# Kernel optimization log

Hardware: AMD Instinct MI355X
Metric: run time of the kernel (lower is better)

## Reference

```python
import jax, jax.numpy as jnp
import numpy as np

B, S, D, H, HD, L, VOCAB, EXP = 32, 744, 512, 8, 64, 4, 1000, 4
EPS = 1e-5


def make_pe(seq_len, d):
    # pe[pos, i]   = sin(pos / 10000**(2*i/d))      (i even)
    # pe[pos, i+1] = cos(pos / 10000**(2*(i+1)/d))  (i even)
    pe = np.zeros((seq_len, d), dtype=np.float32)
    pos = np.arange(seq_len, dtype=np.float32)[:, None]
    i = np.arange(0, d, 2, dtype=np.float32)
    pe[:, 0::2] = np.sin(pos / np.power(10000.0, 2.0 * i / d))
    pe[:, 1::2] = np.cos(pos / np.power(10000.0, 2.0 * (i + 1.0) / d))
    return jnp.asarray(pe)


def setup_inputs() -> dict:
    key = jax.random.key(0)
    ks = jax.random.split(key, 12)
    s = 0.02
    return {
        "x": jax.random.randint(ks[0], (1, B, S), 0, VOCAB, dtype=jnp.int64)
            if jax.config.jax_enable_x64 else jax.random.randint(ks[0], (1, B, S), 0, VOCAB, dtype=jnp.int32),
        "emb": jax.random.normal(ks[1], (VOCAB, D), jnp.float32) * s,
        "pe": make_pe(S, D),
        "Wq": jax.random.normal(ks[2], (L, HD, HD), jnp.float32) * s,
        "Wk": jax.random.normal(ks[3], (L, HD, HD), jnp.float32) * s,
        "Wv": jax.random.normal(ks[4], (L, HD, HD), jnp.float32) * s,
        "Wo": jax.random.normal(ks[5], (L, D, D), jnp.float32) * s,
        "bo": jnp.zeros((L, D), jnp.float32),
        "ln1_w": jnp.ones((L, D), jnp.float32),
        "ln1_b": jnp.zeros((L, D), jnp.float32),
        "W1": jax.random.normal(ks[6], (L, EXP * D, D), jnp.float32) * s,
        "b1": jnp.zeros((L, EXP * D), jnp.float32),
        "W2": jax.random.normal(ks[7], (L, D, EXP * D), jnp.float32) * s,
        "b2": jnp.zeros((L, D), jnp.float32),
        "ln2_w": jnp.ones((L, D), jnp.float32),
        "ln2_b": jnp.zeros((L, D), jnp.float32),
    }


def _layer_norm(x, w, b):
    m = jnp.mean(x, axis=-1, keepdims=True)
    v = jnp.mean(jnp.square(x - m), axis=-1, keepdims=True)
    return (x - m) * jax.lax.rsqrt(v + EPS) * w + b


def _block(h, Wq, Wk, Wv, Wo, bo, g1, be1, W1, bf1, W2, bf2, g2, be2):
    # h: [B, S, D]
    x4 = h.reshape(B, S, H, HD)
    # per-head Linear(64,64, bias=False): y = x @ W.T
    q = jnp.einsum('bshd,ed->bhse', x4, Wq)  # [B,H,S,HD]
    k = jnp.einsum('bshd,ed->bhse', x4, Wk)
    v = jnp.einsum('bshd,ed->bhse', x4, Wv)
    scores = jnp.einsum('bhse,bhte->bhst', q, k) / jnp.sqrt(jnp.float32(HD))
    att = jax.nn.softmax(scores, axis=-1)
    o = jnp.einsum('bhst,bhte->bshe', att, v).reshape(B, S, D)
    o = o @ Wo.T + bo
    # residual uses `value` == h (pre-attention input)
    n1 = _layer_norm(o + h, g1, be1)  # dropout is identity in eval
    ff = jax.nn.relu(n1 @ W1.T + bf1) @ W2.T + bf2
    return _layer_norm(ff + n1, g2, be2)


def reference(x, emb, pe, Wq, Wk, Wv, Wo, bo, ln1_w, ln1_b, W1, b1, W2, b2, ln2_w, ln2_b):
    # embedding + [0, ...] -> [B, S, D]
    h = emb[x][0]
    h = h * jnp.sqrt(jnp.float32(D)) + pe  # pe broadcast over batch
    for l in range(L):
        h = _block(h, Wq[l], Wk[l], Wv[l], Wo[l], bo[l],
                   ln1_w[l], ln1_b[l], W1[l], b1[l], W2[l], b2[l],
                   ln2_w[l], ln2_b[l])
    return h
```

## Files before the change

kernel.cpp:

```cpp
#include <hip/hip_runtime.h>
#include <hip/hip_bf16.h>
#include <math.h>

#define BB 32
#define SS 744
#define DD 512
#define HH 8
#define HDD 64
#define LL 4
#define EXPAND 4
#define NROWS (BB * SS)
#define MROWS (NROWS * HH)
#define NBUF ((size_t)NROWS * DD)
#define SQRT_D 22.62741699796952f
#define QSCALE 0.18033688011112042f
#define VTS 768

typedef __hip_bfloat16 bf16;
typedef __attribute__((ext_vector_type(8))) __bf16 bf16x8;
typedef __attribute__((ext_vector_type(4))) float f32x4;

#define GPTR(p) (const __attribute__((address_space(1))) void*)(p)
#define LPTR(p) (__attribute__((address_space(3))) void*)(p)


__global__ __launch_bounds__(128) void k_embed(const int* __restrict__ x,
                                               const float* __restrict__ emb,
                                               const float* __restrict__ pe,
                                               float* __restrict__ h,
                                               bf16* __restrict__ h16) {
    int row = blockIdx.x;
    int s = row % SS;
    int tok = x[row];
    int t = threadIdx.x;
    float4 e = ((const float4*)(emb + (size_t)tok * DD))[t];
    float4 p = ((const float4*)(pe + (size_t)s * DD))[t];
    float4 o;
    o.x = e.x * SQRT_D + p.x;
    o.y = e.y * SQRT_D + p.y;
    o.z = e.z * SQRT_D + p.z;
    o.w = e.w * SQRT_D + p.w;
    ((float4*)(h + (size_t)row * DD))[t] = o;
    bf16 b0 = __float2bfloat16(o.x), b1 = __float2bfloat16(o.y);
    bf16 b2 = __float2bfloat16(o.z), b3 = __float2bfloat16(o.w);
    ushort4 u;
    u.x = *(unsigned short*)&b0; u.y = *(unsigned short*)&b1;
    u.z = *(unsigned short*)&b2; u.w = *(unsigned short*)&b3;
    ((ushort4*)(h16 + (size_t)row * DD))[t] = u;
}

__global__ __launch_bounds__(256) void k_f2b(const float* __restrict__ in,
                                             bf16* __restrict__ out, int n) {
    for (int i = blockIdx.x * 256 + threadIdx.x; i < n; i += gridDim.x * 256)
        out[i] = __float2bfloat16(in[i]);
}

__global__ __launch_bounds__(256) void k_qkv_mfma(const bf16* __restrict__ A,
                                                  const bf16* __restrict__ Wqkv,
                                                  bf16* __restrict__ qk,
                                                  bf16* __restrict__ v) {
    __shared__ __align__(16) bf16 As[2][128][32];
    __shared__ __align__(16) bf16 Ws[2][192][32];
    int t = threadIdx.x;
    int w = t >> 6, lane = t & 63;
    int fr = lane & 15, fq = lane >> 4;
    int m0 = blockIdx.x * 128;
    int wm = (w >> 1) * 64;
    int wc = (w & 1) * 96;
    int lr = lane >> 2;
    int csw = ((lane & 3) ^ ((lane >> 3) & 3)) * 8;
    int swz8 = (fq ^ ((fr >> 1) & 3)) * 8;

#pragma unroll
    for (int kc = 0; kc < 2; kc++)
#pragma unroll
        for (int i = 0; i < 2; i++) {
            int rb = w * 32 + i * 16;
            __builtin_amdgcn_global_load_lds(
                GPTR(A + (size_t)(m0 + rb + lr) * 64 + kc * 32 + csw),
                LPTR(&As[kc][rb][0]), 16, 0, 0);
        }
#pragma unroll
    for (int kc = 0; kc < 2; kc++)
#pragma unroll
        for (int i = 0; i < 3; i++) {
            int rb = w * 48 + i * 16;
            __builtin_amdgcn_global_load_lds(
                GPTR(Wqkv + (size_t)(rb + lr) * 64 + kc * 32 + csw),
                LPTR(&Ws[kc][rb][0]), 16, 0, 0);
        }
    __syncthreads();

    bf16x8 af[2][4], bw[2][6];
#pragma unroll
    for (int kc = 0; kc < 2; kc++) {
#pragma unroll
        for (int mi = 0; mi < 4; mi++)
            af[kc][mi] = *(const bf16x8*)&As[kc][wm + mi * 16 + fr][swz8];
#pragma unroll
        for (int ni = 0; ni < 6; ni++)
            bw[kc][ni] = *(const bf16x8*)&Ws[kc][wc + ni * 16 + fr][swz8];
    }
    f32x4 acc[4][6] = {};
#pragma unroll
    for (int mi = 0; mi < 4; mi++)
#pragma unroll
        for (int ni = 0; ni < 6; ni++) {
            acc[mi][ni] = __builtin_amdgcn_mfma_f32_16x16x32_bf16(af[0][mi], bw[0][ni], acc[mi][ni], 0, 0, 0);
            acc[mi][ni] = __builtin_amdgcn_mfma_f32_16x16x32_bf16(af[1][mi], bw[1][ni], acc[mi][ni], 0, 0, 0);
        }

#pragma unroll
    for (int mi = 0; mi < 4; mi++)
#pragma unroll
        for (int r = 0; r < 4; r++) {
            size_t mg = m0 + wm + mi * 16 + fq * 4 + r;
#pragma unroll
            for (int ni = 0; ni < 6; ni++) {
                int col = wc + ni * 16 + fr;
                float fv = acc[mi][ni][r];
                if (col < 64) fv *= QSCALE;
                bf16 val = __float2bfloat16(fv);
                if (col < 128) qk[mg * 128 + col] = val;
                else           v[mg * 64 + (col - 128)] = val;
            }
        }
}

__global__ __launch_bounds__(256) void k_vt(const bf16* __restrict__ v,
                                            bf16* __restrict__ vt) {
    int bh = blockIdx.x, st = blockIdx.y;
    int b = bh >> 3, h = bh & 7;
    int t = threadIdx.x;
    __shared__ bf16 Ls[64][72];
    int s0 = st * 64;
    for (int j = t; j < 512; j += 256) {
        int si = j >> 3, e8 = (j & 7) * 8;
        int s = s0 + si; if (s > SS - 1) s = SS - 1;
        bf16x8 val = *(const bf16x8*)(v + ((size_t)(b * SS + s) * 8 + h) * 64 + e8);
        *(bf16x8*)&Ls[si][e8] = val;
    }
    __syncthreads();
    for (int j = t; j < 512; j += 256) {
        int d = j >> 3, o8 = (j & 7) * 8;
        int half = o8 & 32, fqv = (o8 & 31) >> 3;
        __align__(16) bf16 tmp[8];
#pragma unroll
        for (int i = 0; i < 8; i++)
            tmp[i] = Ls[half + 4 * fqv + 16 * (i >> 2) + (i & 3)][d];
        *(bf16x8*)(vt + ((size_t)bh * 64 + d) * VTS + s0 + o8) = *(bf16x8*)tmp;
    }
}

__global__ __launch_bounds__(256) void k_attn_mfma(const bf16* __restrict__ qk,
                                                   const bf16* __restrict__ vt,
                                                   bf16* __restrict__ ao) {
    int bh = blockIdx.x, qt = blockIdx.y;
    int b = bh >> 3, h = bh & 7;
    int t = threadIdx.x;
    int w = t >> 6, lane = t & 63;
    int fr = lane & 15, fq = lane >> 4;
    int lr = lane >> 2;
    int csw = ((lane & 3) ^ ((lane >> 3) & 3)) * 8;
    int swz8 = (fq ^ ((fr >> 1) & 3)) * 8;
    int q0 = qt * 128;

    __shared__ __align__(16) bf16 Ks[2][2][64][32];
    __shared__ __align__(16) bf16 Vs[2][2][64][32];

    bf16x8 qf[2][2];
#pragma unroll
    for (int qs = 0; qs < 2; qs++) {
        int row = q0 + w * 32 + qs * 16 + fr;
        if (row > SS - 1) row = SS - 1;
        size_t gb = ((size_t)(b * SS + row) * 8 + h) * 128;
        qf[qs][0] = *(const bf16x8*)(qk + gb + fq * 8);
        qf[qs][1] = *(const bf16x8*)(qk + gb + 32 + fq * 8);
    }

    f32x4 o_acc[2][4] = {};
    float l_[2] = {0.f, 0.f};

    auto STAGE = [&](int buf, int kt) {
        int k0 = kt * 64;
        int krow = k0 + w * 16 + lr; if (krow > SS - 1) krow = SS - 1;
        size_t kgb = ((size_t)(b * SS + krow) * 8 + h) * 128 + 64;
        size_t vgb = ((size_t)bh * 64 + w * 16 + lr) * VTS + k0;
#pragma unroll
        for (int p = 0; p < 2; p++) {
            __builtin_amdgcn_global_load_lds(GPTR(qk + kgb + p * 32 + csw),
                                             LPTR(&Ks[buf][p][w * 16][0]), 16, 0, 0);
            __builtin_amdgcn_global_load_lds(GPTR(vt + vgb + p * 32 + csw),
                                             LPTR(&Vs[buf][p][w * 16][0]), 16, 0, 0);
        }
    };

    STAGE(0, 0);
    for (int kt = 0; kt < 12; kt++) {
        int cur = kt & 1;
        __syncthreads();
        if (kt < 11) STAGE(cur ^ 1, kt + 1);

        bf16x8 kf[4][2];
#pragma unroll
        for (int n = 0; n < 4; n++) {
            kf[n][0] = *(const bf16x8*)&Ks[cur][0][n * 16 + fr][swz8];
            kf[n][1] = *(const bf16x8*)&Ks[cur][1][n * 16 + fr][swz8];
        }

        bf16x8 pf[2][2];
#pragma unroll
        for (int qs = 0; qs < 2; qs++) {
            f32x4 st[4] = {};
            __builtin_amdgcn_s_setprio(1);
#pragma unroll
            for (int n = 0; n < 4; n++) {
                st[n] = __builtin_amdgcn_mfma_f32_16x16x32_bf16(kf[n][0], qf[qs][0], st[n], 0, 0, 0);
                st[n] = __builtin_amdgcn_mfma_f32_16x16x32_bf16(kf[n][1], qf[qs][1], st[n], 0, 0, 0);
            }
            __builtin_amdgcn_s_setprio(0);
            if (kt == 11) {
#pragma unroll
                for (int n = 0; n < 4; n++) {
                    int kb = 704 + n * 16 + fq * 4;
#pragma unroll
                    for (int r = 0; r < 4; r++)
                        if (kb + r >= SS) st[n][r] = -1e30f;
                }
            }
            float ls = 0.f;
#pragma unroll
            for (int n = 0; n < 4; n++)
#pragma unroll
                for (int r = 0; r < 4; r++) {
                    float p = exp2f(st[n][r]);
                    st[n][r] = p;
                    ls += p;
                }
            l_[qs] += ls;
            bf16x8 t0, t1;
#pragma unroll
            for (int e = 0; e < 4; e++) {
                t0[e]     = (__bf16)st[0][e];
                t0[e + 4] = (__bf16)st[1][e];
                t1[e]     = (__bf16)st[2][e];
                t1[e + 4] = (__bf16)st[3][e];
            }
            pf[qs][0] = t0;
            pf[qs][1] = t1;
        }

        __builtin_amdgcn_s_setprio(1);
#pragma unroll
        for (int dt = 0; dt < 4; dt++) {
            bf16x8 vf0 = *(const bf16x8*)&Vs[cur][0][dt * 16 + fr][swz8];
            bf16x8 vf1 = *(const bf16x8*)&Vs[cur][1][dt * 16 + fr][swz8];
#pragma unroll
            for (int qs = 0; qs < 2; qs++) {
                o_acc[qs][dt] = __builtin_amdgcn_mfma_f32_16x16x32_bf16(vf0, pf[qs][0], o_acc[qs][dt], 0, 0, 0);
                o_acc[qs][dt] = __builtin_amdgcn_mfma_f32_16x16x32_bf16(vf1, pf[qs][1], o_acc[qs][dt], 0, 0, 0);
            }
        }
        __builtin_amdgcn_s_setprio(0);
    }

#pragma unroll
    for (int qs = 0; qs < 2; qs++) {
        int srow = q0 + w * 32 + qs * 16 + fr;
        if (srow < SS) {
            float lt = l_[qs];
            lt += __shfl_xor(lt, 16);
            lt += __shfl_xor(lt, 32);
            float inv = 1.f / lt;
            bf16* dst = ao + ((size_t)(b * SS + srow) * 8 + h) * 64;
#pragma unroll
            for (int dt = 0; dt < 4; dt++) {
                __align__(8) bf16 tb[4];
#pragma unroll
                for (int r = 0; r < 4; r++)
                    tb[r] = __float2bfloat16(o_acc[qs][dt][r] * inv);
                *(unsigned long long*)(dst + dt * 16 + fq * 4) =
                    *(unsigned long long*)tb;
            }
        }
    }
}

template <bool RELU, bool OUT_BF16>
__global__ __launch_bounds__(256) void k_gemm_mfma(const bf16* __restrict__ A,
                                                   const bf16* __restrict__ W,
                                                   const float* __restrict__ bias,
                                                   void* __restrict__ Cout,
                                                   int M, int N, int K) {
    __shared__ __align__(16) bf16 As[128 * 32];
    __shared__ __align__(16) bf16 Ws[128 * 32];
    int t = threadIdx.x;
    int wave = t >> 6, lane = t & 63;
    int m0 = blockIdx.x * 128, n0 = blockIdx.y * 128;
    int wm = (wave >> 1) * 64, wn = (wave & 1) * 64;
    int fr = lane & 15, fq = lane >> 4;
    int csw = ((lane & 3) ^ ((lane >> 3) & 3)) * 8;
    int swz8 = (fq ^ ((fr >> 1) & 3)) * 8;

    f32x4 acc[4][4] = {};

    int r0 = wave * 16 + (lane >> 2);
    int r1 = r0 + 64;

    for (int k0 = 0; k0 < K; k0 += 32) {
        __syncthreads();
        __builtin_amdgcn_global_load_lds(GPTR(A + (size_t)(m0 + r0) * K + k0 + csw),
                                         LPTR((char*)As + (wave << 10)), 16, 0, 0);
        __builtin_amdgcn_global_load_lds(GPTR(A + (size_t)(m0 + r1) * K + k0 + csw),
                                         LPTR((char*)As + (wave << 10) + 4096), 16, 0, 0);
        __builtin_amdgcn_global_load_lds(GPTR(W + (size_t)(n0 + r0) * K + k0 + csw),
                                         LPTR((char*)Ws + (wave << 10)), 16, 0, 0);
        __builtin_amdgcn_global_load_lds(GPTR(W + (size_t)(n0 + r1) * K + k0 + csw),
                                         LPTR((char*)Ws + (wave << 10) + 4096), 16, 0, 0);
        __syncthreads();

        bf16x8 af[4], bfr[4];
#pragma unroll
        for (int i = 0; i < 4; i++)
            af[i] = *(const bf16x8*)(As + (wm + i * 16 + fr) * 32 + swz8);
#pragma unroll
        for (int i = 0; i < 4; i++)
            bfr[i] = *(const bf16x8*)(Ws + (wn + i * 16 + fr) * 32 + swz8);
#pragma unroll
        for (int mi = 0; mi < 4; mi++)
#pragma unroll
            for (int ni = 0; ni < 4; ni++)
                acc[mi][ni] = __builtin_amdgcn_mfma_f32_16x16x32_bf16(
                    af[mi], bfr[ni], acc[mi][ni], 0, 0, 0);
    }

    float bv[4];
#pragma unroll
    for (int ni = 0; ni < 4; ni++) bv[ni] = bias[n0 + wn + ni * 16 + fr];
#pragma unroll
    for (int mi = 0; mi < 4; mi++) {
#pragma unroll
        for (int r = 0; r < 4; r++) {
            int mg = m0 + wm + mi * 16 + fq * 4 + r;
#pragma unroll
            for (int ni = 0; ni < 4; ni++) {
                float val = acc[mi][ni][r] + bv[ni];
                if (RELU) val = fmaxf(val, 0.f);
                int ng = n0 + wn + ni * 16 + fr;
                if (OUT_BF16)
                    ((bf16*)Cout)[(size_t)mg * N + ng] = __float2bfloat16(val);
                else
                    ((float*)Cout)[(size_t)mg * N + ng] = val;
            }
        }
    }
}

template <bool BRES16, bool WF32>
__global__ __launch_bounds__(128) void k_add_ln(const float* __restrict__ a,
                                                const void* __restrict__ bres,
                                                const float* __restrict__ w,
                                                const float* __restrict__ bias,
                                                float* out,
                                                bf16* __restrict__ out16) {
    int row = blockIdx.x;
    int t = threadIdx.x;
    float4 xa = ((const float4*)(a + (size_t)row * DD))[t];
    float4 xb;
    if (BRES16) {
        ushort4 ub = ((const ushort4*)((const bf16*)bres + (size_t)row * DD))[t];
        xb.x = __bfloat162float(*(bf16*)&ub.x);
        xb.y = __bfloat162float(*(bf16*)&ub.y);
        xb.z = __bfloat162float(*(bf16*)&ub.z);
        xb.w = __bfloat162float(*(bf16*)&ub.w);
    } else {
        xb = ((const float4*)((const float*)bres + (size_t)row * DD))[t];
    }
    float4 vv;
    vv.x = xa.x + xb.x; vv.y = xa.y + xb.y;
    vv.z = xa.z + xb.z; vv.w = xa.w + xb.w;
    float s  = vv.x + vv.y + vv.z + vv.w;
    float sq = vv.x * vv.x + vv.y * vv.y + vv.z * vv.z + vv.w * vv.w;
#pragma unroll
    for (int off = 32; off > 0; off >>= 1) {
        s  += __shfl_down(s, off);
        sq += __shfl_down(sq, off);
    }
    __shared__ float red[4];
    if ((t & 63) == 0) { red[(t >> 6) * 2] = s; red[(t >> 6) * 2 + 1] = sq; }
    __syncthreads();
    float S1 = red[0] + red[2], S2 = red[1] + red[3];
    float mean = S1 * (1.f / DD);
    float var  = S2 * (1.f / DD) - mean * mean;
    float inv  = rsqrtf(var + 1e-5f);
    float4 wv = ((const float4*)w)[t];
    float4 bv = ((const float4*)bias)[t];
    float4 o;
    o.x = (vv.x - mean) * inv * wv.x + bv.x;
    o.y = (vv.y - mean) * inv * wv.y + bv.y;
    o.z = (vv.z - mean) * inv * wv.z + bv.z;
    o.w = (vv.w - mean) * inv * wv.w + bv.w;
    if (WF32)
        ((float4*)(out + (size_t)row * DD))[t] = o;
    bf16 h0 = __float2bfloat16(o.x), h1 = __float2bfloat16(o.y);
    bf16 h2 = __float2bfloat16(o.z), h3 = __float2bfloat16(o.w);
    ushort4 u;
    u.x = *(unsigned short*)&h0; u.y = *(unsigned short*)&h1;
    u.z = *(unsigned short*)&h2; u.w = *(unsigned short*)&h3;
    ((ushort4*)(out16 + (size_t)row * DD))[t] = u;
}

extern "C" void kernel_launch(void* const* d_in, const int* in_sizes, int n_in,
                              void* d_out, int out_size, void* d_ws, size_t ws_size,
                              hipStream_t stream) {
    const int*   x    = (const int*)d_in[0];
    const float* emb  = (const float*)d_in[1];
    const float* pe   = (const float*)d_in[2];
    const float* Wq   = (const float*)d_in[3];
    const float* Wk   = (const float*)d_in[4];
    const float* Wv   = (const float*)d_in[5];
    const float* Wo   = (const float*)d_in[6];
    const float* bo   = (const float*)d_in[7];
    const float* ln1w = (const float*)d_in[8];
    const float* ln1b = (const float*)d_in[9];
    const float* W1   = (const float*)d_in[10];
    const float* b1   = (const float*)d_in[11];
    const float* W2   = (const float*)d_in[12];
    const float* b2   = (const float*)d_in[13];
    const float* ln2w = (const float*)d_in[14];
    const float* ln2b = (const float*)d_in[15];

    float* h  = (float*)d_out;
    float* ws = (float*)d_ws;
    bf16*  qkbuf  = (bf16*)ws;
    float* wo_out = ws;
    float* ff     = ws;
    bf16*  v_buf  = (bf16*)(ws + NBUF);
    bf16*  vt_buf = (bf16*)(ws + NBUF + NBUF / 2);
    bf16*  wqkv   = vt_buf;
    bf16*  f1b    = (bf16*)(ws + NBUF);
    bf16*  regD   = (bf16*)(ws + 3 * NBUF);
    bf16*  h16    = regD + NBUF;
    bf16*  wob16  = h16 + NBUF;
    bf16*  w1b16  = wob16 + (size_t)LL * DD * DD;
    bf16*  w2b16  = w1b16 + (size_t)LL * EXPAND * DD * DD;

    k_f2b<<<2048, 256, 0, stream>>>(Wo, wob16, LL * DD * DD);
    k_f2b<<<4096, 256, 0, stream>>>(W1, w1b16, LL * EXPAND * DD * DD);
    k_f2b<<<4096, 256, 0, stream>>>(W2, w2b16, LL * EXPAND * DD * DD);
    k_embed<<<NROWS, 128, 0, stream>>>(x, emb, pe, h, h16);

    for (int l = 0; l < LL; l++) {
        k_f2b<<<16, 256, 0, stream>>>(Wq + (size_t)l * 4096, wqkv, 4096);
        k_f2b<<<16, 256, 0, stream>>>(Wk + (size_t)l * 4096, wqkv + 4096, 4096);
        k_f2b<<<16, 256, 0, stream>>>(Wv + (size_t)l * 4096, wqkv + 8192, 4096);
        k_qkv_mfma<<<MROWS / 128, 256, 0, stream>>>(h16, wqkv, qkbuf, v_buf);
        k_vt<<<dim3(256, 12), 256, 0, stream>>>(v_buf, vt_buf);
        k_attn_mfma<<<dim3(256, 6), 256, 0, stream>>>(qkbuf, vt_buf, regD);
        k_gemm_mfma<false, false><<<dim3(NROWS / 128, DD / 128), 256, 0, stream>>>(
            regD, wob16 + (size_t)l * DD * DD, bo + (size_t)l * DD, wo_out,
            NROWS, DD, DD);
        k_add_ln<false, false><<<NROWS, 128, 0, stream>>>(wo_out, h,
            ln1w + (size_t)l * DD, ln1b + (size_t)l * DD, nullptr, regD);
        k_gemm_mfma<true, true><<<dim3(NROWS / 128, (EXPAND * DD) / 128), 256, 0, stream>>>(
            regD, w1b16 + (size_t)l * EXPAND * DD * DD, b1 + (size_t)l * EXPAND * DD,
            f1b, NROWS, EXPAND * DD, DD);
        k_gemm_mfma<false, false><<<dim3(NROWS / 128, DD / 128), 256, 0, stream>>>(
            f1b, w2b16 + (size_t)l * DD * EXPAND * DD, b2 + (size_t)l * DD,
            ff, NROWS, DD, EXPAND * DD);
        k_add_ln<true, true><<<NROWS, 128, 0, stream>>>(ff, regD,
            ln2w + (size_t)l * DD, ln2b + (size_t)l * DD, h, h16);
    }
}
```

Baseline: 1.484 ms.

## Double-buffer GEMM LDS tiles, XCD-swizzle block order, fuse QKV weight conversion

The bf16 MFMA GEMM now keeps two LDS buffers for the A and W tiles. It issues the next k-tile's global-to-LDS loads before computing on the current one, so each iteration needs one barrier instead of two. The grid is transposed and block IDs are remapped in strides of 8, so that consecutive blocks on the same XCD share row or column tiles for better L2 reuse. The three per-layer Wq/Wk/Wv bf16 conversion launches are merged into one kernel. The cost is twice the LDS per block, which may lower occupancy, and the remap assumes the block count is divisible by 8.

```diff
diff --git a/kernel.cpp b/kernel.cpp
--- a/kernel.cpp
+++ b/kernel.cpp
@@ -55,6 +55,16 @@
         out[i] = __float2bfloat16(in[i]);
 }
 
+__global__ __launch_bounds__(256) void k_qkvw(const float* __restrict__ q,
+                                              const float* __restrict__ k,
+                                              const float* __restrict__ v,
+                                              bf16* __restrict__ out) {
+    int i = blockIdx.x * 256 + threadIdx.x;
+    out[i]        = __float2bfloat16(q[i]);
+    out[i + 4096] = __float2bfloat16(k[i]);
+    out[i + 8192] = __float2bfloat16(v[i]);
+}
+
 __global__ __launch_bounds__(256) void k_qkv_mfma(const bf16* __restrict__ A,
                                                   const bf16* __restrict__ Wqkv,
                                                   bf16* __restrict__ qk,
@@ -292,11 +302,17 @@
                                                    const float* __restrict__ bias,
                                                    void* __restrict__ Cout,
                                                    int M, int N, int K) {
-    __shared__ __align__(16) bf16 As[128 * 32];
-    __shared__ __align__(16) bf16 Ws[128 * 32];
+    __shared__ __align__(16) bf16 As[2][128 * 32];
+    __shared__ __align__(16) bf16 Ws[2][128 * 32];
     int t = threadIdx.x;
     int wave = t >> 6, lane = t & 63;
-    int m0 = blockIdx.x * 128, n0 = blockIdx.y * 128;
+    int nbx = gridDim.x;
+    int nwg = nbx * gridDim.y;
+    int bid = blockIdx.y * nbx + blockIdx.x;
+    int cpx = nwg >> 3;
+    int swz = (bid & 7) * cpx + (bid >> 3);
+    int n0 = (swz % nbx) * 128;
+    int m0 = (swz / nbx) * 128;
     int wm = (wave >> 1) * 64, wn = (wave & 1) * 64;
     int fr = lane & 15, fq = lane >> 4;
     int csw = ((lane & 3) ^ ((lane >> 3) & 3)) * 8;
@@ -307,25 +323,31 @@
     int r0 = wave * 16 + (lane >> 2);
     int r1 = r0 + 64;
 
-    for (int k0 = 0; k0 < K; k0 += 32) {
+    auto STAGE = [&](int buf, int k0) {
+        __builtin_amdgcn_global_load_lds(GPTR(A + (size_t)(m0 + r0) * K + k0 + csw),
+                                         LPTR((char*)&As[buf][0] + (wave << 10)), 16, 0, 0);
+        __builtin_amdgcn_global_load_lds(GPTR(A + (size_t)(m0 + r1) * K + k0 + csw),
+                                         LPTR((char*)&As[buf][0] + (wave << 10) + 4096), 16, 0, 0);
+        __builtin_amdgcn_global_load_lds(GPTR(W + (size_t)(n0 + r0) * K + k0 + csw),
+                                         LPTR((char*)&Ws[buf][0] + (wave << 10)), 16, 0, 0);
+        __builtin_amdgcn_global_load_lds(GPTR(W + (size_t)(n0 + r1) * K + k0 + csw),
+                                         LPTR((char*)&Ws[buf][0] + (wave << 10) + 4096), 16, 0, 0);
+    };
+
+    int nk = K >> 5;
+    STAGE(0, 0);
+    for (int kt = 0; kt < nk; kt++) {
+        int cur = kt & 1;
         __syncthreads();
-        __builtin_amdgcn_global_load_lds(GPTR(A + (size_t)(m0 + r0) * K + k0 + csw),
-                                         LPTR((char*)As + (wave << 10)), 16, 0, 0);
-        __builtin_amdgcn_global_load_lds(GPTR(A + (size_t)(m0 + r1) * K + k0 + csw),
-                                         LPTR((char*)As + (wave << 10) + 4096), 16, 0, 0);
-        __builtin_amdgcn_global_load_lds(GPTR(W + (size_t)(n0 + r0) * K + k0 + csw),
-                                         LPTR((char*)Ws + (wave << 10)), 16, 0, 0);
-        __builtin_amdgcn_global_load_lds(GPTR(W + (size_t)(n0 + r1) * K + k0 + csw),
-                                         LPTR((char*)Ws + (wave << 10) + 4096), 16, 0, 0);
-        __syncthreads();
+        if (kt + 1 < nk) STAGE(cur ^ 1, (kt + 1) << 5);
 
         bf16x8 af[4], bfr[4];
 #pragma unroll
         for (int i = 0; i < 4; i++)
-            af[i] = *(const bf16x8*)(As + (wm + i * 16 + fr) * 32 + swz8);
+            af[i] = *(const bf16x8*)(&As[cur][0] + (wm + i * 16 + fr) * 32 + swz8);
 #pragma unroll
         for (int i = 0; i < 4; i++)
-            bfr[i] = *(const bf16x8*)(Ws + (wn + i * 16 + fr) * 32 + swz8);
+            bfr[i] = *(const bf16x8*)(&Ws[cur][0] + (wn + i * 16 + fr) * 32 + swz8);
 #pragma unroll
         for (int mi = 0; mi < 4; mi++)
 #pragma unroll
@@ -451,21 +473,20 @@
     k_embed<<<NROWS, 128, 0, stream>>>(x, emb, pe, h, h16);
 
     for (int l = 0; l < LL; l++) {
-        k_f2b<<<16, 256, 0, stream>>>(Wq + (size_t)l * 4096, wqkv, 4096);
-        k_f2b<<<16, 256, 0, stream>>>(Wk + (size_t)l * 4096, wqkv + 4096, 4096);
-        k_f2b<<<16, 256, 0, stream>>>(Wv + (size_t)l * 4096, wqkv + 8192, 4096);
+        k_qkvw<<<16, 256, 0, stream>>>(Wq + (size_t)l * 4096, Wk + (size_t)l * 4096,
+                                       Wv + (size_t)l * 4096, wqkv);
         k_qkv_mfma<<<MROWS / 128, 256, 0, stream>>>(h16, wqkv, qkbuf, v_buf);
         k_vt<<<dim3(256, 12), 256, 0, stream>>>(v_buf, vt_buf);
         k_attn_mfma<<<dim3(256, 6), 256, 0, stream>>>(qkbuf, vt_buf, regD);
-        k_gemm_mfma<false, false><<<dim3(NROWS / 128, DD / 128), 256, 0, stream>>>(
+        k_gemm_mfma<false, false><<<dim3(DD / 128, NROWS / 128), 256, 0, stream>>>(
             regD, wob16 + (size_t)l * DD * DD, bo + (size_t)l * DD, wo_out,
             NROWS, DD, DD);
         k_add_ln<false, false><<<NROWS, 128, 0, stream>>>(wo_out, h,
             ln1w + (size_t)l * DD, ln1b + (size_t)l * DD, nullptr, regD);
-        k_gemm_mfma<true, true><<<dim3(NROWS / 128, (EXPAND * DD) / 128), 256, 0, stream>>>(
+        k_gemm_mfma<true, true><<<dim3((EXPAND * DD) / 128, NROWS / 128), 256, 0, stream>>>(
             regD, w1b16 + (size_t)l * EXPAND * DD * DD, b1 + (size_t)l * EXPAND * DD,
             f1b, NROWS, EXPAND * DD, DD);
-        k_gemm_mfma<false, false><<<dim3(NROWS / 128, DD / 128), 256, 0, stream>>>(
+        k_gemm_mfma<false, false><<<dim3(DD / 128, NROWS / 128), 256, 0, stream>>>(
             f1b, w2b16 + (size_t)l * DD * EXPAND * DD, b2 + (size_t)l * DD,
             ff, NROWS, DD, EXPAND * DD);
         k_add_ln<true, true><<<NROWS, 128, 0, stream>>>(ff, regD,
```

Measured after the change: 1.294 ms. 1.15x faster.
